# Performance work log

Hardware: AMD Instinct MI355X
Metric: run time of the kernel (lower is better)

The kernel has to match this reference:

```python
import jax, jax.numpy as jnp
import numpy as np

D = 256; NH = 8; DH = D // NH; NL = 4; NP = 4; DFFN = 1024
SPATIAL = [(128, 128), (64, 64), (32, 32), (16, 16)]
LEN_IN = sum(h * w for h, w in SPATIAL)
N, LQ = 8, 1000


def _ln(x, g, b, eps=1e-5):
    m = jnp.mean(x, -1, keepdims=True)
    v = jnp.mean((x - m) ** 2, -1, keepdims=True)
    return (x - m) * jax.lax.rsqrt(v + eps) * g + b


def _ms_deform_core(value, loc, attn_w):
    # value (N,Len_in,NH,DH); loc (N,Lq,NH,NL,NP,2) in [0,1]; attn_w (N,Lq,NH,NL,NP)
    n, lq = loc.shape[0], loc.shape[1]
    out = jnp.zeros((n, NH, lq, DH), value.dtype)
    start = 0
    for l, (Hl, Wl) in enumerate(SPATIAL):
        v = value[:, start:start + Hl * Wl].transpose(0, 2, 1, 3)  # (N,NH,HW,DH)
        start += Hl * Wl
        # grid_sample-style mapping, align_corners=False, zero padding
        x = loc[:, :, :, l, :, 0] * Wl - 0.5  # (N,Lq,NH,NP)
        y = loc[:, :, :, l, :, 1] * Hl - 0.5
        x0 = jnp.floor(x); y0 = jnp.floor(y)
        lx = x - x0; ly = y - y0
        x0i = x0.astype(jnp.int32); y0i = y0.astype(jnp.int32)
        acc = jnp.zeros((n, NH, lq, NP, DH), value.dtype)
        for dy, dx, w in ((0, 0, (1 - ly) * (1 - lx)), (0, 1, (1 - ly) * lx),
                          (1, 0, ly * (1 - lx)), (1, 1, ly * lx)):
            xi = x0i + dx; yi = y0i + dy
            valid = ((xi >= 0) & (xi < Wl) & (yi >= 0) & (yi < Hl)).astype(value.dtype)
            idx = jnp.clip(yi, 0, Hl - 1) * Wl + jnp.clip(xi, 0, Wl - 1)  # (N,Lq,NH,NP)
            idx = idx.transpose(0, 2, 1, 3).reshape(n, NH, lq * NP)
            g = jnp.take_along_axis(v, idx[..., None], axis=2).reshape(n, NH, lq, NP, DH)
            acc = acc + g * (w * valid).transpose(0, 2, 1, 3)[..., None]
        out = out + jnp.sum(acc * attn_w[:, :, :, l].transpose(0, 2, 1, 3)[..., None], axis=3)
    return out.transpose(0, 2, 1, 3).reshape(n, lq, D)


def setup_inputs() -> dict:
    key = jax.random.key(0)
    ks = jax.random.split(key, 16)
    s = 0.02
    inp = {
        'tgt': jax.random.normal(ks[0], (N, LQ, D), jnp.float32),
        'query_pos': jax.random.normal(ks[1], (N, LQ, D), jnp.float32),
        'reference_points': jax.random.uniform(ks[2], (N, LQ, NL, 2), jnp.float32),
        'src': jax.random.normal(ks[3], (N, LEN_IN, D), jnp.float32),
        'spatial_shapes': jnp.array(SPATIAL, jnp.int32),
        'level_start_index': jnp.array(np.cumsum([0] + [h * w for h, w in SPATIAL[:-1]]), jnp.int32),
        # self-attention
        'sa_in_w': jax.random.normal(ks[4], (3 * D, D), jnp.float32) * s,
        'sa_in_b': jnp.zeros((3 * D,), jnp.float32),
        'sa_out_w': jax.random.normal(ks[5], (D, D), jnp.float32) * s,
        'sa_out_b': jnp.zeros((D,), jnp.float32),
        'norm2_g': jnp.ones((D,), jnp.float32), 'norm2_b': jnp.zeros((D,), jnp.float32),
        # MSDeformAttn
        'off_w': jax.random.normal(ks[6], (NH * NL * NP * 2, D), jnp.float32) * s,
        'off_b': jax.random.normal(ks[7], (NH * NL * NP * 2,), jnp.float32) * s,
        'aw_w': jax.random.normal(ks[8], (NH * NL * NP, D), jnp.float32) * s,
        'aw_b': jnp.zeros((NH * NL * NP,), jnp.float32),
        'val_w': jax.random.normal(ks[9], (D, D), jnp.float32) * s,
        'val_b': jnp.zeros((D,), jnp.float32),
        'outp_w': jax.random.normal(ks[10], (D, D), jnp.float32) * s,
        'outp_b': jnp.zeros((D,), jnp.float32),
        'norm1_g': jnp.ones((D,), jnp.float32), 'norm1_b': jnp.zeros((D,), jnp.float32),
        # FFN
        'ffn_w1': jax.random.normal(ks[11], (DFFN, D), jnp.float32) * s,
        'ffn_b1': jnp.zeros((DFFN,), jnp.float32),
        'ffn_w2': jax.random.normal(ks[12], (D, DFFN), jnp.float32) * s,
        'ffn_b2': jnp.zeros((D,), jnp.float32),
        'norm3_g': jnp.ones((D,), jnp.float32), 'norm3_b': jnp.zeros((D,), jnp.float32),
    }
    return inp


def reference(tgt, query_pos, reference_points, src, spatial_shapes, level_start_index,
              sa_in_w, sa_in_b, sa_out_w, sa_out_b, norm2_g, norm2_b,
              off_w, off_b, aw_w, aw_b, val_w, val_b, outp_w, outp_b, norm1_g, norm1_b,
              ffn_w1, ffn_b1, ffn_w2, ffn_b2, norm3_g, norm3_b):
    n, lq, _ = tgt.shape
    # ---- self-attention (q = k = tgt + pos, v = tgt), eval mode (dropout off)
    qk = tgt + query_pos
    wq, wk, wv = sa_in_w[:D], sa_in_w[D:2 * D], sa_in_w[2 * D:]
    bq, bk, bv = sa_in_b[:D], sa_in_b[D:2 * D], sa_in_b[2 * D:]
    q = (qk @ wq.T + bq).reshape(n, lq, NH, DH)
    k = (qk @ wk.T + bk).reshape(n, lq, NH, DH)
    v = (tgt @ wv.T + bv).reshape(n, lq, NH, DH)
    scores = jnp.einsum('bqhd,bkhd->bhqk', q, k) / np.sqrt(DH).astype(np.float32)
    attn = jax.nn.softmax(scores, axis=-1)
    sa = jnp.einsum('bhqk,bkhd->bqhd', attn, v).reshape(n, lq, D) @ sa_out_w.T + sa_out_b
    tgt = _ln(tgt + sa, norm2_g, norm2_b)
    # ---- multi-scale deformable cross-attention
    query = tgt + query_pos
    value = (src @ val_w.T + val_b).reshape(n, LEN_IN, NH, DH)
    offsets = (query @ off_w.T + off_b).reshape(n, lq, NH, NL, NP, 2)
    aw = (query @ aw_w.T + aw_b).reshape(n, lq, NH, NL * NP)
    aw = jax.nn.softmax(aw, axis=-1).reshape(n, lq, NH, NL, NP)
    # offset normalizer: (W_l, H_l)
    norm = jnp.stack([spatial_shapes[:, 1], spatial_shapes[:, 0]], -1).astype(tgt.dtype)
    loc = reference_points[:, :, None, :, None, :] + offsets / norm[None, None, None, :, None, :]
    ca = _ms_deform_core(value, loc, aw) @ outp_w.T + outp_b
    tgt = _ln(tgt + ca, norm1_g, norm1_b)
    # ---- FFN
    ff = jax.nn.relu(tgt @ ffn_w1.T + ffn_b1) @ ffn_w2.T + ffn_b2
    tgt = _ln(tgt + ff, norm3_g, norm3_b)
    return tgt
```

## Files before the change

kernel.cpp:

```cpp
#include <hip/hip_runtime.h>
#include <hip/hip_bf16.h>

#define D 256
#define NH 8
#define DH 32
#define NL 4
#define NP 4
#define DFFN 1024
#define LEN_IN 21760
#define NB 8
#define LQ 1000

typedef __hip_bfloat16 bf16;
typedef __attribute__((ext_vector_type(8))) short s8v;
typedef __attribute__((ext_vector_type(4))) float f4v;

__device__ inline float toF(float x) { return x; }
__device__ inline float toF(bf16 x) { return __bfloat162float(x); }

template <typename T> __device__ inline T fromF(float x);
template <> __device__ inline float fromF<float>(float x) { return x; }
template <> __device__ inline bf16 fromF<bf16>(float x) { return __float2bfloat16(x); }

__device__ inline short bfr(float f) {
    unsigned u = __float_as_uint(f);
    u += 0x7fff + ((u >> 16) & 1);
    return (short)(u >> 16);
}
__device__ inline s8v pack8(float4 x, float4 y) {
    s8v r;
    r[0] = bfr(x.x); r[1] = bfr(x.y); r[2] = bfr(x.z); r[3] = bfr(x.w);
    r[4] = bfr(y.x); r[5] = bfr(y.y); r[6] = bfr(y.z); r[7] = bfr(y.w);
    return r;
}

template <typename TA, typename TC>
__global__ __launch_bounds__(256) void mfma_gemm(const TA* __restrict__ A, const float* __restrict__ A2,
                                                 const float* __restrict__ W, const float* __restrict__ bias,
                                                 TC* __restrict__ C, int M, int N, int K, int do_relu) {
    constexpr int LDT = 40;
    __shared__ bf16 As[128 * LDT];
    __shared__ bf16 Bs[128 * LDT];
    const int tid = threadIdx.x;
    const int m0 = blockIdx.y * 128, n0 = blockIdx.x * 128;
    const int srow = tid >> 1;
    const int sks = (tid & 1) * 16;
    const int lane = tid & 63;
    const int wave = tid >> 6;
    const int wm = (wave >> 1) * 64, wn = (wave & 1) * 64;
    const int fr = lane & 15, fq = lane >> 4;

    int arow = m0 + srow; if (arow >= M) arow = M - 1;
    const TA* aptr = A + (size_t)arow * K + sks;
    const float* a2ptr = A2 ? (A2 + (size_t)arow * K + sks) : nullptr;
    const float* wptr = W + (size_t)(n0 + srow) * K + sks;

    f4v acc[4][4];
#pragma unroll
    for (int i = 0; i < 4; ++i)
#pragma unroll
        for (int j = 0; j < 4; ++j) acc[i][j] = (f4v){0.f, 0.f, 0.f, 0.f};

    for (int k0 = 0; k0 < K; k0 += 32) {
        s8v av0, av1, wv0, wv1;
        if constexpr (sizeof(TA) == 2) {
            av0 = *(const s8v*)((const bf16*)aptr + k0);
            av1 = *(const s8v*)((const bf16*)aptr + k0 + 8);
        } else {
            float4 a0 = *(const float4*)(aptr + k0);
            float4 a1 = *(const float4*)(aptr + k0 + 4);
            float4 a2 = *(const float4*)(aptr + k0 + 8);
            float4 a3 = *(const float4*)(aptr + k0 + 12);
            if (a2ptr) {
                float4 b0 = *(const float4*)(a2ptr + k0);
                float4 b1 = *(const float4*)(a2ptr + k0 + 4);
                float4 b2 = *(const float4*)(a2ptr + k0 + 8);
                float4 b3 = *(const float4*)(a2ptr + k0 + 12);
                a0.x += b0.x; a0.y += b0.y; a0.z += b0.z; a0.w += b0.w;
                a1.x += b1.x; a1.y += b1.y; a1.z += b1.z; a1.w += b1.w;
                a2.x += b2.x; a2.y += b2.y; a2.z += b2.z; a2.w += b2.w;
                a3.x += b3.x; a3.y += b3.y; a3.z += b3.z; a3.w += b3.w;
            }
            av0 = pack8(a0, a1);
            av1 = pack8(a2, a3);
        }
        {
            float4 w0 = *(const float4*)(wptr + k0);
            float4 w1 = *(const float4*)(wptr + k0 + 4);
            float4 w2 = *(const float4*)(wptr + k0 + 8);
            float4 w3 = *(const float4*)(wptr + k0 + 12);
            wv0 = pack8(w0, w1);
            wv1 = pack8(w2, w3);
        }
        __syncthreads();
        *(s8v*)&As[srow * LDT + sks] = av0;
        *(s8v*)&As[srow * LDT + sks + 8] = av1;
        *(s8v*)&Bs[srow * LDT + sks] = wv0;
        *(s8v*)&Bs[srow * LDT + sks + 8] = wv1;
        __syncthreads();
        s8v af[4], bfv[4];
#pragma unroll
        for (int i = 0; i < 4; ++i) af[i] = *(s8v*)&As[(wm + i * 16 + fr) * LDT + fq * 8];
#pragma unroll
        for (int j = 0; j < 4; ++j) bfv[j] = *(s8v*)&Bs[(wn + j * 16 + fr) * LDT + fq * 8];
#pragma unroll
        for (int i = 0; i < 4; ++i)
#pragma unroll
            for (int j = 0; j < 4; ++j)
                acc[i][j] = __builtin_amdgcn_mfma_f32_16x16x32_bf16(af[i], bfv[j], acc[i][j], 0, 0, 0);
    }

#pragma unroll
    for (int i = 0; i < 4; ++i) {
        int rbase = m0 + wm + i * 16 + fq * 4;
#pragma unroll
        for (int r = 0; r < 4; ++r) {
            int row = rbase + r;
            if (row < M) {
#pragma unroll
                for (int j = 0; j < 4; ++j) {
                    int col = n0 + wn + j * 16 + fr;
                    float v = acc[i][j][r] + bias[col];
                    if (do_relu) v = fmaxf(v, 0.f);
                    C[(size_t)row * N + col] = fromF<TC>(v);
                }
            }
        }
    }
}

__global__ __launch_bounds__(256) void attn_mfma(const float* __restrict__ q, const float* __restrict__ k,
                                                 const float* __restrict__ v, float* __restrict__ out) {
    const int h = blockIdx.y, n = blockIdx.z;
    const int tid = threadIdx.x, wave = tid >> 6, lane = tid & 63;
    const int fr = lane & 15, fq = lane >> 4;
    __shared__ short Ks[32 * 40];
    __shared__ short Vt[32 * 40];
    __shared__ short Pl[4][16 * 40];
    const int q0 = blockIdx.x * 64 + wave * 16;

    s8v qfrag;
    {
        int qr = q0 + fr; if (qr >= LQ) qr = LQ - 1;
        const float* qp = q + ((size_t)(n * LQ + qr)) * D + h * DH + fq * 8;
        float4 t0 = *(const float4*)qp;
        float4 t1 = *(const float4*)(qp + 4);
        const float sc = 0.17677669529663687f;
        t0.x *= sc; t0.y *= sc; t0.z *= sc; t0.w *= sc;
        t1.x *= sc; t1.y *= sc; t1.z *= sc; t1.w *= sc;
        qfrag = pack8(t0, t1);
    }

    f4v O0 = {0.f, 0.f, 0.f, 0.f}, O1 = {0.f, 0.f, 0.f, 0.f};
    float mrow[4] = {-1e30f, -1e30f, -1e30f, -1e30f};
    float lrow[4] = {0.f, 0.f, 0.f, 0.f};

    for (int kt = 0; kt < LQ; kt += 32) {
        __syncthreads();
        {
            int key = tid >> 3, d4 = (tid & 7) * 4;
            int gk = kt + key; if (gk >= LQ) gk = LQ - 1;
            const float* kp = k + ((size_t)(n * LQ + gk)) * D + h * DH + d4;
            float4 t = *(const float4*)kp;
            short4 pk; pk.x = bfr(t.x); pk.y = bfr(t.y); pk.z = bfr(t.z); pk.w = bfr(t.w);
            *(short4*)&Ks[key * 40 + d4] = pk;
        }
        {
            int d = tid & 31, key0 = (tid >> 5) * 4;
            float vv[4];
#pragma unroll
            for (int i = 0; i < 4; ++i) {
                int gk = kt + key0 + i; if (gk >= LQ) gk = LQ - 1;
                vv[i] = v[((size_t)(n * LQ + gk)) * D + h * DH + d];
            }
            short4 pk; pk.x = bfr(vv[0]); pk.y = bfr(vv[1]); pk.z = bfr(vv[2]); pk.w = bfr(vv[3]);
            *(short4*)&Vt[d * 40 + key0] = pk;
        }
        __syncthreads();

        f4v s0 = {0.f, 0.f, 0.f, 0.f}, s1 = {0.f, 0.f, 0.f, 0.f};
        s8v kf0 = *(s8v*)&Ks[fr * 40 + fq * 8];
        s8v kf1 = *(s8v*)&Ks[(16 + fr) * 40 + fq * 8];
        s0 = __builtin_amdgcn_mfma_f32_16x16x32_bf16(qfrag, kf0, s0, 0, 0, 0);
        s1 = __builtin_amdgcn_mfma_f32_16x16x32_bf16(qfrag, kf1, s1, 0, 0, 0);
        const bool val0 = (kt + fr) < LQ, val1 = (kt + 16 + fr) < LQ;

        float p0[4], p1[4], alpha[4];
#pragma unroll
        for (int r = 0; r < 4; ++r) {
            float a = val0 ? s0[r] : -1e30f;
            float b = val1 ? s1[r] : -1e30f;
            float mx = fmaxf(a, b);
            mx = fmaxf(mx, __shfl_xor(mx, 1, 64));
            mx = fmaxf(mx, __shfl_xor(mx, 2, 64));
            mx = fmaxf(mx, __shfl_xor(mx, 4, 64));
            mx = fmaxf(mx, __shfl_xor(mx, 8, 64));
            float mnew = fmaxf(mrow[r], mx);
            float al = __expf(mrow[r] - mnew);
            float e0 = __expf(a - mnew);
            float e1 = __expf(b - mnew);
            float ps = e0 + e1;
            ps += __shfl_xor(ps, 1, 64);
            ps += __shfl_xor(ps, 2, 64);
            ps += __shfl_xor(ps, 4, 64);
            ps += __shfl_xor(ps, 8, 64);
            lrow[r] = lrow[r] * al + ps;
            mrow[r] = mnew;
            alpha[r] = al;
            p0[r] = e0; p1[r] = e1;
        }

        short* pw = Pl[wave];
#pragma unroll
        for (int r = 0; r < 4; ++r) {
            pw[(fq * 4 + r) * 40 + fr] = bfr(p0[r]);
            pw[(fq * 4 + r) * 40 + 16 + fr] = bfr(p1[r]);
        }
        __builtin_amdgcn_s_waitcnt(0);
        s8v pfrag = *(s8v*)&pw[fr * 40 + fq * 8];
        s8v vf0 = *(s8v*)&Vt[fr * 40 + fq * 8];
        s8v vf1 = *(s8v*)&Vt[(16 + fr) * 40 + fq * 8];
#pragma unroll
        for (int r = 0; r < 4; ++r) { O0[r] *= alpha[r]; O1[r] *= alpha[r]; }
        O0 = __builtin_amdgcn_mfma_f32_16x16x32_bf16(pfrag, vf0, O0, 0, 0, 0);
        O1 = __builtin_amdgcn_mfma_f32_16x16x32_bf16(pfrag, vf1, O1, 0, 0, 0);
    }

#pragma unroll
    for (int r = 0; r < 4; ++r) {
        int qrow = q0 + fq * 4 + r;
        if (qrow < LQ) {
            float inv = 1.0f / lrow[r];
            float* op = out + ((size_t)(n * LQ + qrow)) * D + h * DH;
            op[fr] = O0[r] * inv;
            op[16 + fr] = O1[r] * inv;
        }
    }
}

__global__ __launch_bounds__(256) void ln_res_kernel(const float* __restrict__ base, const float* __restrict__ delta,
                                                     const float* __restrict__ g, const float* __restrict__ b,
                                                     float* __restrict__ out) {
    __shared__ float scratch[8];
    const size_t row = blockIdx.x;
    const int d = threadIdx.x;
    float x = base[row * D + d] + delta[row * D + d];
    float s1 = x, s2 = x * x;
    for (int o = 32; o > 0; o >>= 1) {
        s1 += __shfl_down(s1, o, 64);
        s2 += __shfl_down(s2, o, 64);
    }
    const int w = threadIdx.x >> 6, lane = threadIdx.x & 63;
    if (lane == 0) { scratch[w] = s1; scratch[4 + w] = s2; }
    __syncthreads();
    s1 = scratch[0] + scratch[1] + scratch[2] + scratch[3];
    s2 = scratch[4] + scratch[5] + scratch[6] + scratch[7];
    float mean = s1 * (1.0f / 256.0f);
    float var = s2 * (1.0f / 256.0f) - mean * mean;
    float rstd = rsqrtf(var + 1e-5f);
    float y = (x - mean) * rstd * g[d] + b[d];
    out[row * D + d] = y;
}

__global__ __launch_bounds__(256) void aw_softmax_kernel(float* __restrict__ aw, int ngrp) {
    int t = blockIdx.x * 256 + threadIdx.x;
    if (t >= ngrp) return;
    float* p = aw + (size_t)t * 16;
    float m = p[0];
#pragma unroll
    for (int i = 1; i < 16; ++i) m = fmaxf(m, p[i]);
    float s = 0.f;
    float e[16];
#pragma unroll
    for (int i = 0; i < 16; ++i) { e[i] = __expf(p[i] - m); s += e[i]; }
    float inv = 1.0f / s;
#pragma unroll
    for (int i = 0; i < 16; ++i) p[i] = e[i] * inv;
}

__global__ __launch_bounds__(256) void deform_kernel(const bf16* __restrict__ value, const float* __restrict__ offs,
                                                     const float* __restrict__ aw, const float* __restrict__ refp,
                                                     float* __restrict__ out) {
    const int h = blockIdx.y, n = blockIdx.z;
    const int tid = threadIdx.x;
    const int wave = tid >> 6, lane = tid & 63;
    const int qi = blockIdx.x * 4 + wave;
    const int c = lane & 15;
    const int l = lane >> 4;
    const size_t row = (size_t)n * LQ + qi;
    const int W = 128 >> l, H = 128 >> l;
    const int START[4] = {0, 16384, 20480, 21504};
    const float invW = 1.0f / W, invH = 1.0f / H;

    const float rx = refp[(row * NL + l) * 2 + 0];
    const float ry = refp[(row * NL + l) * 2 + 1];
    const bf16* vbase = value + ((size_t)n * LEN_IN + START[l]) * D + h * DH + 2 * c;
    const float* offp = offs + row * D + (h * NL + l) * NP * 2;
    const float* awp = aw + row * 128 + h * 16 + l * 4;

    float acc0 = 0.f, acc1 = 0.f;
#pragma unroll
    for (int p = 0; p < 4; ++p) {
        float ox = offp[p * 2 + 0];
        float oy = offp[p * 2 + 1];
        float wa = awp[p];
        float x = (rx + ox * invW) * W - 0.5f;
        float y = (ry + oy * invH) * H - 0.5f;
        float xf = floorf(x), yf = floorf(y);
        float lx = x - xf, ly = y - yf;
        int x0 = (int)xf, y0 = (int)yf;
        int x1 = x0 + 1, y1 = y0 + 1;
        float vx0 = (x0 >= 0 && x0 < W) ? 1.f : 0.f;
        float vx1 = (x1 >= 0 && x1 < W) ? 1.f : 0.f;
        float vy0 = (y0 >= 0 && y0 < H) ? 1.f : 0.f;
        float vy1 = (y1 >= 0 && y1 < H) ? 1.f : 0.f;
        int x0c = min(max(x0, 0), W - 1), x1c = min(max(x1, 0), W - 1);
        int y0c = min(max(y0, 0), H - 1), y1c = min(max(y1, 0), H - 1);
        float w00 = wa * (1.f - ly) * (1.f - lx) * vy0 * vx0;
        float w01 = wa * (1.f - ly) * lx * vy0 * vx1;
        float w10 = wa * ly * (1.f - lx) * vy1 * vx0;
        float w11 = wa * ly * lx * vy1 * vx1;
        unsigned u00 = *(const unsigned*)(vbase + (size_t)(y0c * W + x0c) * D);
        unsigned u01 = *(const unsigned*)(vbase + (size_t)(y0c * W + x1c) * D);
        unsigned u10 = *(const unsigned*)(vbase + (size_t)(y1c * W + x0c) * D);
        unsigned u11 = *(const unsigned*)(vbase + (size_t)(y1c * W + x1c) * D);
        acc0 += w00 * __uint_as_float(u00 << 16) + w01 * __uint_as_float(u01 << 16)
              + w10 * __uint_as_float(u10 << 16) + w11 * __uint_as_float(u11 << 16);
        acc1 += w00 * __uint_as_float(u00 & 0xffff0000u) + w01 * __uint_as_float(u01 & 0xffff0000u)
              + w10 * __uint_as_float(u10 & 0xffff0000u) + w11 * __uint_as_float(u11 & 0xffff0000u);
    }
    acc0 += __shfl_xor(acc0, 16, 64); acc0 += __shfl_xor(acc0, 32, 64);
    acc1 += __shfl_xor(acc1, 16, 64); acc1 += __shfl_xor(acc1, 32, 64);
    if (l == 0) {
        float2 st = {acc0, acc1};
        *(float2*)(out + row * D + h * DH + 2 * c) = st;
    }
}

extern "C" void kernel_launch(void* const* d_in, const int* in_sizes, int n_in,
                              void* d_out, int out_size, void* d_ws, size_t ws_size,
                              hipStream_t stream) {
    const float* tgt = (const float*)d_in[0];
    const float* qpos = (const float*)d_in[1];
    const float* refp = (const float*)d_in[2];
    const float* src = (const float*)d_in[3];
    const float* sa_in_w = (const float*)d_in[6];
    const float* sa_in_b = (const float*)d_in[7];
    const float* sa_out_w = (const float*)d_in[8];
    const float* sa_out_b = (const float*)d_in[9];
    const float* norm2_g = (const float*)d_in[10];
    const float* norm2_b = (const float*)d_in[11];
    const float* off_w = (const float*)d_in[12];
    const float* off_b = (const float*)d_in[13];
    const float* aw_w = (const float*)d_in[14];
    const float* aw_b = (const float*)d_in[15];
    const float* val_w = (const float*)d_in[16];
    const float* val_b = (const float*)d_in[17];
    const float* outp_w = (const float*)d_in[18];
    const float* outp_b = (const float*)d_in[19];
    const float* norm1_g = (const float*)d_in[20];
    const float* norm1_b = (const float*)d_in[21];
    const float* ffn_w1 = (const float*)d_in[22];
    const float* ffn_b1 = (const float*)d_in[23];
    const float* ffn_w2 = (const float*)d_in[24];
    const float* ffn_b2 = (const float*)d_in[25];
    const float* norm3_g = (const float*)d_in[26];
    const float* norm3_b = (const float*)d_in[27];
    float* outp = (float*)d_out;

    const size_t NTOK = (size_t)NB * LQ;
    const size_t NE = NTOK * D;
    float* w = (float*)d_ws;
    size_t off = 0;
    auto alloc = [&](size_t n) { float* p = w + off; off += n; return p; };
    float* bufA = alloc(NE);
    float* bufB = alloc(NE);
    float* bufC = alloc(NE);
    float* bufD = alloc(NE);
    float* tgt2 = alloc(NE);
    float* tgt3 = alloc(NE);
    float* awb = alloc(NTOK * 128);
    bf16* mid = (bf16*)alloc(NTOK * DFFN / 2);
    bf16* value = (bf16*)(w + off);

    const int M8K = (int)NTOK;
    dim3 gD(2, (M8K + 127) / 128);

    mfma_gemm<float, float><<<gD, 256, 0, stream>>>(tgt, qpos, sa_in_w, sa_in_b, bufB, M8K, D, D, 0);
    mfma_gemm<float, float><<<gD, 256, 0, stream>>>(tgt, qpos, sa_in_w + 256 * 256, sa_in_b + 256, bufC, M8K, D, D, 0);
    mfma_gemm<float, float><<<gD, 256, 0, stream>>>(tgt, nullptr, sa_in_w + 512 * 256, sa_in_b + 512, bufD, M8K, D, D, 0);
    attn_mfma<<<dim3((LQ + 63) / 64, NH, NB), 256, 0, stream>>>(bufB, bufC, bufD, bufA);
    mfma_gemm<float, float><<<gD, 256, 0, stream>>>(bufA, nullptr, sa_out_w, sa_out_b, bufB, M8K, D, D, 0);
    ln_res_kernel<<<NTOK, 256, 0, stream>>>(tgt, bufB, norm2_g, norm2_b, tgt2);

    mfma_gemm<float, bf16><<<dim3(2, (NB * LEN_IN) / 128), 256, 0, stream>>>(src, nullptr, val_w, val_b, value,
                                                                             NB * LEN_IN, D, D, 0);
    mfma_gemm<float, float><<<gD, 256, 0, stream>>>(tgt2, qpos, off_w, off_b, bufD, M8K, D, D, 0);
    mfma_gemm<float, float><<<dim3(1, (M8K + 127) / 128), 256, 0, stream>>>(tgt2, qpos, aw_w, aw_b, awb, M8K, 128, D, 0);
    aw_softmax_kernel<<<(int)(NTOK * NH + 255) / 256, 256, 0, stream>>>(awb, (int)(NTOK * NH));
    deform_kernel<<<dim3(LQ / 4, NH, NB), 256, 0, stream>>>(value, bufD, awb, refp, bufA);
    mfma_gemm<float, float><<<gD, 256, 0, stream>>>(bufA, nullptr, outp_w, outp_b, bufB, M8K, D, D, 0);
    ln_res_kernel<<<NTOK, 256, 0, stream>>>(tgt2, bufB, norm1_g, norm1_b, tgt3);

    mfma_gemm<float, bf16><<<dim3(DFFN / 128, (M8K + 127) / 128), 256, 0, stream>>>(tgt3, nullptr, ffn_w1, ffn_b1,
                                                                                    mid, M8K, DFFN, D, 1);
    mfma_gemm<bf16, float><<<gD, 256, 0, stream>>>(mid, nullptr, ffn_w2, ffn_b2, bufC, M8K, D, DFFN, 0);
    ln_res_kernel<<<NTOK, 256, 0, stream>>>(tgt3, bufC, norm3_g, norm3_b, outp);
}
```

Baseline: 691.2 us.

## Pre-pack weights to bf16 and replace LDS-tiled GEMM with direct-load MFMA GEMM

A new kernel converts all fp32 weight matrices to bf16 in one launch at the start of the forward pass. The GEMM kernel is rewritten to load A and W fragments straight from global memory into MFMA registers, with no shared-memory staging or barriers. It uses a hardware packed bf16 convert and smaller 64-row tiles so more blocks launch. This removes LDS traffic and syncs, but gives up on-chip data reuse and drops the M-bound guards, relying on M being a multiple of 64.

```diff
diff --git a/kernel.cpp b/kernel.cpp
--- a/kernel.cpp
+++ b/kernel.cpp
@@ -15,9 +15,6 @@
 typedef __attribute__((ext_vector_type(8))) short s8v;
 typedef __attribute__((ext_vector_type(4))) float f4v;
 
-__device__ inline float toF(float x) { return x; }
-__device__ inline float toF(bf16 x) { return __bfloat162float(x); }
-
 template <typename T> __device__ inline T fromF(float x);
 template <> __device__ inline float fromF<float>(float x) { return x; }
 template <> __device__ inline bf16 fromF<bf16>(float x) { return __float2bfloat16(x); }
@@ -34,96 +31,112 @@
     return r;
 }
 
-template <typename TA, typename TC>
-__global__ __launch_bounds__(256) void mfma_gemm(const TA* __restrict__ A, const float* __restrict__ A2,
-                                                 const float* __restrict__ W, const float* __restrict__ bias,
-                                                 TC* __restrict__ C, int M, int N, int K, int do_relu) {
-    constexpr int LDT = 40;
-    __shared__ bf16 As[128 * LDT];
-    __shared__ bf16 Bs[128 * LDT];
+__device__ inline unsigned cvtpk(float a, float b) {
+    unsigned r;
+    asm("v_cvt_pk_bf16_f32 %0, %1, %2" : "=v"(r) : "v"(a), "v"(b));
+    return r;
+}
+__device__ inline s8v pkcvt8(float4 a, float4 b) {
+    union { s8v v; unsigned u[4]; } r;
+    r.u[0] = cvtpk(a.x, a.y);
+    r.u[1] = cvtpk(a.z, a.w);
+    r.u[2] = cvtpk(b.x, b.y);
+    r.u[3] = cvtpk(b.z, b.w);
+    return r.v;
+}
+
+__global__ __launch_bounds__(256) void pack_weights(const float* __restrict__ s0, const float* __restrict__ s1,
+                                                    const float* __restrict__ s2, const float* __restrict__ s3,
+                                                    const float* __restrict__ s4, const float* __restrict__ s5,
+                                                    const float* __restrict__ s6, const float* __restrict__ s7,
+                                                    bf16* __restrict__ dst) {
+    int g = blockIdx.x * 256 + threadIdx.x;
+    const float* s; int base;
+    if      (g <  49152) { s = s0; base = 0;      }
+    else if (g <  65536) { s = s1; base = 49152;  }
+    else if (g <  81920) { s = s2; base = 65536;  }
+    else if (g <  90112) { s = s3; base = 81920;  }
+    else if (g < 106496) { s = s4; base = 90112;  }
+    else if (g < 122880) { s = s5; base = 106496; }
+    else if (g < 188416) { s = s6; base = 122880; }
+    else                 { s = s7; base = 188416; }
+    float4 v = ((const float4*)s)[g - base];
+    short4 o; o.x = bfr(v.x); o.y = bfr(v.y); o.z = bfr(v.z); o.w = bfr(v.w);
+    ((short4*)dst)[g] = o;
+}
+
+template <typename TA, typename TC, int MT, bool ADD2>
+__global__ __launch_bounds__(256) void gemm_direct(const TA* __restrict__ A, const float* __restrict__ A2,
+                                                   const bf16* __restrict__ W, const float* __restrict__ bias,
+                                                   TC* __restrict__ C, int M, int N, int K, int do_relu) {
     const int tid = threadIdx.x;
-    const int m0 = blockIdx.y * 128, n0 = blockIdx.x * 128;
-    const int srow = tid >> 1;
-    const int sks = (tid & 1) * 16;
-    const int lane = tid & 63;
-    const int wave = tid >> 6;
-    const int wm = (wave >> 1) * 64, wn = (wave & 1) * 64;
+    const int lane = tid & 63, wave = tid >> 6;
     const int fr = lane & 15, fq = lane >> 4;
-
-    int arow = m0 + srow; if (arow >= M) arow = M - 1;
-    const TA* aptr = A + (size_t)arow * K + sks;
-    const float* a2ptr = A2 ? (A2 + (size_t)arow * K + sks) : nullptr;
-    const float* wptr = W + (size_t)(n0 + srow) * K + sks;
-
-    f4v acc[4][4];
-#pragma unroll
-    for (int i = 0; i < 4; ++i)
+    const int n0 = blockIdx.x * 128;
+    const int wrow = blockIdx.y * (MT * 32) + (wave >> 1) * (MT * 16);
+    const int wn = n0 + (wave & 1) * 64;
+    (void)M;
+
+    const TA* ap[MT];
+    const float* a2p[MT];
+#pragma unroll
+    for (int i = 0; i < MT; ++i) {
+        size_t r = (size_t)(wrow + i * 16 + fr);
+        ap[i] = A + r * K + fq * 8;
+        if constexpr (ADD2) a2p[i] = A2 + r * K + fq * 8;
+    }
+    const bf16* wp[4];
+#pragma unroll
+    for (int j = 0; j < 4; ++j) wp[j] = W + (size_t)(wn + j * 16 + fr) * K + fq * 8;
+
+    f4v acc[MT][4];
+#pragma unroll
+    for (int i = 0; i < MT; ++i)
 #pragma unroll
         for (int j = 0; j < 4; ++j) acc[i][j] = (f4v){0.f, 0.f, 0.f, 0.f};
 
     for (int k0 = 0; k0 < K; k0 += 32) {
-        s8v av0, av1, wv0, wv1;
-        if constexpr (sizeof(TA) == 2) {
-            av0 = *(const s8v*)((const bf16*)aptr + k0);
-            av1 = *(const s8v*)((const bf16*)aptr + k0 + 8);
-        } else {
-            float4 a0 = *(const float4*)(aptr + k0);
-            float4 a1 = *(const float4*)(aptr + k0 + 4);
-            float4 a2 = *(const float4*)(aptr + k0 + 8);
-            float4 a3 = *(const float4*)(aptr + k0 + 12);
-            if (a2ptr) {
-                float4 b0 = *(const float4*)(a2ptr + k0);
-                float4 b1 = *(const float4*)(a2ptr + k0 + 4);
-                float4 b2 = *(const float4*)(a2ptr + k0 + 8);
-                float4 b3 = *(const float4*)(a2ptr + k0 + 12);
-                a0.x += b0.x; a0.y += b0.y; a0.z += b0.z; a0.w += b0.w;
-                a1.x += b1.x; a1.y += b1.y; a1.z += b1.z; a1.w += b1.w;
-                a2.x += b2.x; a2.y += b2.y; a2.z += b2.z; a2.w += b2.w;
-                a3.x += b3.x; a3.y += b3.y; a3.z += b3.z; a3.w += b3.w;
+        s8v bfv[4];
+#pragma unroll
+        for (int j = 0; j < 4; ++j) { bfv[j] = *(const s8v*)wp[j]; wp[j] += 32; }
+        s8v af[MT];
+#pragma unroll
+        for (int i = 0; i < MT; ++i) {
+            if constexpr (sizeof(TA) == 2) {
+                af[i] = *(const s8v*)ap[i];
+            } else {
+                float4 x0 = *(const float4*)ap[i];
+                float4 x1 = *(const float4*)(ap[i] + 4);
+                if constexpr (ADD2) {
+                    float4 y0 = *(const float4*)a2p[i];
+                    float4 y1 = *(const float4*)(a2p[i] + 4);
+                    x0.x += y0.x; x0.y += y0.y; x0.z += y0.z; x0.w += y0.w;
+                    x1.x += y1.x; x1.y += y1.y; x1.z += y1.z; x1.w += y1.w;
+                    a2p[i] += 32;
+                }
+                af[i] = pkcvt8(x0, x1);
             }
-            av0 = pack8(a0, a1);
-            av1 = pack8(a2, a3);
-        }
-        {
-            float4 w0 = *(const float4*)(wptr + k0);
-            float4 w1 = *(const float4*)(wptr + k0 + 4);
-            float4 w2 = *(const float4*)(wptr + k0 + 8);
-            float4 w3 = *(const float4*)(wptr + k0 + 12);
-            wv0 = pack8(w0, w1);
-            wv1 = pack8(w2, w3);
-        }
-        __syncthreads();
-        *(s8v*)&As[srow * LDT + sks] = av0;
-        *(s8v*)&As[srow * LDT + sks + 8] = av1;
-        *(s8v*)&Bs[srow * LDT + sks] = wv0;
-        *(s8v*)&Bs[srow * LDT + sks + 8] = wv1;
-        __syncthreads();
-        s8v af[4], bfv[4];
-#pragma unroll
-        for (int i = 0; i < 4; ++i) af[i] = *(s8v*)&As[(wm + i * 16 + fr) * LDT + fq * 8];
-#pragma unroll
-        for (int j = 0; j < 4; ++j) bfv[j] = *(s8v*)&Bs[(wn + j * 16 + fr) * LDT + fq * 8];
-#pragma unroll
-        for (int i = 0; i < 4; ++i)
+            ap[i] += 32;
+        }
+#pragma unroll
+        for (int i = 0; i < MT; ++i)
 #pragma unroll
             for (int j = 0; j < 4; ++j)
                 acc[i][j] = __builtin_amdgcn_mfma_f32_16x16x32_bf16(af[i], bfv[j], acc[i][j], 0, 0, 0);
     }
 
 #pragma unroll
-    for (int i = 0; i < 4; ++i) {
-        int rbase = m0 + wm + i * 16 + fq * 4;
-#pragma unroll
-        for (int r = 0; r < 4; ++r) {
-            int row = rbase + r;
-            if (row < M) {
-#pragma unroll
-                for (int j = 0; j < 4; ++j) {
-                    int col = n0 + wn + j * 16 + fr;
-                    float v = acc[i][j][r] + bias[col];
-                    if (do_relu) v = fmaxf(v, 0.f);
-                    C[(size_t)row * N + col] = fromF<TC>(v);
-                }
+    for (int j = 0; j < 4; ++j) {
+        const int col = wn + j * 16 + fr;
+        const float bb = bias[col];
+#pragma unroll
+        for (int i = 0; i < MT; ++i) {
+            const int rbase = wrow + i * 16 + fq * 4;
+#pragma unroll
+            for (int r = 0; r < 4; ++r) {
+                float v = acc[i][j][r] + bb;
+                if (do_relu) v = fmaxf(v, 0.f);
+                C[(size_t)(rbase + r) * N + col] = fromF<TC>(v);
             }
         }
     }
@@ -381,29 +394,45 @@
     float* tgt3 = alloc(NE);
     float* awb = alloc(NTOK * 128);
     bf16* mid = (bf16*)alloc(NTOK * DFFN / 2);
-    bf16* value = (bf16*)(w + off);
+    bf16* value = (bf16*)alloc((size_t)NB * LEN_IN * D / 2);
+    bf16* wb = (bf16*)alloc(507904);
+
+    const bf16* wq    = wb;
+    const bf16* wk    = wb + 65536;
+    const bf16* wv    = wb + 131072;
+    const bf16* wo    = wb + 196608;
+    const bf16* woff  = wb + 262144;
+    const bf16* waw   = wb + 327680;
+    const bf16* wval  = wb + 360448;
+    const bf16* woutp = wb + 425984;
+    const bf16* wf1   = wb + 491520;
+    const bf16* wf2   = wb + 753664;
 
     const int M8K = (int)NTOK;
-    dim3 gD(2, (M8K + 127) / 128);
-
-    mfma_gemm<float, float><<<gD, 256, 0, stream>>>(tgt, qpos, sa_in_w, sa_in_b, bufB, M8K, D, D, 0);
-    mfma_gemm<float, float><<<gD, 256, 0, stream>>>(tgt, qpos, sa_in_w + 256 * 256, sa_in_b + 256, bufC, M8K, D, D, 0);
-    mfma_gemm<float, float><<<gD, 256, 0, stream>>>(tgt, nullptr, sa_in_w + 512 * 256, sa_in_b + 512, bufD, M8K, D, D, 0);
+    dim3 g8(2, M8K / 64);
+    dim3 g8aw(1, M8K / 64);
+    dim3 g8f1(DFFN / 128, M8K / 64);
+    dim3 gVal(2, (NB * LEN_IN) / 128);
+
+    pack_weights<<<992, 256, 0, stream>>>(sa_in_w, sa_out_w, off_w, aw_w, val_w, outp_w, ffn_w1, ffn_w2, wb);
+
+    gemm_direct<float, float, 2, true><<<g8, 256, 0, stream>>>(tgt, qpos, wq, sa_in_b, bufB, M8K, D, D, 0);
+    gemm_direct<float, float, 2, true><<<g8, 256, 0, stream>>>(tgt, qpos, wk, sa_in_b + 256, bufC, M8K, D, D, 0);
+    gemm_direct<float, float, 2, false><<<g8, 256, 0, stream>>>(tgt, nullptr, wv, sa_in_b + 512, bufD, M8K, D, D, 0);
     attn_mfma<<<dim3((LQ + 63) / 64, NH, NB), 256, 0, stream>>>(bufB, bufC, bufD, bufA);
-    mfma_gemm<float, float><<<gD, 256, 0, stream>>>(bufA, nullptr, sa_out_w, sa_out_b, bufB, M8K, D, D, 0);
+    gemm_direct<float, float, 2, false><<<g8, 256, 0, stream>>>(bufA, nullptr, wo, sa_out_b, bufB, M8K, D, D, 0);
     ln_res_kernel<<<NTOK, 256, 0, stream>>>(tgt, bufB, norm2_g, norm2_b, tgt2);
 
-    mfma_gemm<float, bf16><<<dim3(2, (NB * LEN_IN) / 128), 256, 0, stream>>>(src, nullptr, val_w, val_b, value,
-                                                                             NB * LEN_IN, D, D, 0);
-    mfma_gemm<float, float><<<gD, 256, 0, stream>>>(tgt2, qpos, off_w, off_b, bufD, M8K, D, D, 0);
-    mfma_gemm<float, float><<<dim3(1, (M8K + 127) / 128), 256, 0, stream>>>(tgt2, qpos, aw_w, aw_b, awb, M8K, 128, D, 0);
+    gemm_direct<float, bf16, 4, false><<<gVal, 256, 0, stream>>>(src, nullptr, wval, val_b, value,
+                                                                 NB * LEN_IN, D, D, 0);
+    gemm_direct<float, float, 2, true><<<g8, 256, 0, stream>>>(tgt2, qpos, woff, off_b, bufD, M8K, D, D, 0);
+    gemm_direct<float, float, 2, true><<<g8aw, 256, 0, stream>>>(tgt2, qpos, waw, aw_b, awb, M8K, 128, D, 0);
     aw_softmax_kernel<<<(int)(NTOK * NH + 255) / 256, 256, 0, stream>>>(awb, (int)(NTOK * NH));
     deform_kernel<<<dim3(LQ / 4, NH, NB), 256, 0, stream>>>(value, bufD, awb, refp, bufA);
-    mfma_gemm<float, float><<<gD, 256, 0, stream>>>(bufA, nullptr, outp_w, outp_b, bufB, M8K, D, D, 0);
+    gemm_direct<float, float, 2, false><<<g8, 256, 0, stream>>>(bufA, nullptr, woutp, outp_b, bufB, M8K, D, D, 0);
     ln_res_kernel<<<NTOK, 256, 0, stream>>>(tgt2, bufB, norm1_g, norm1_b, tgt3);
 
-    mfma_gemm<float, bf16><<<dim3(DFFN / 128, (M8K + 127) / 128), 256, 0, stream>>>(tgt3, nullptr, ffn_w1, ffn_b1,
-                                                                                    mid, M8K, DFFN, D, 1);
-    mfma_gemm<bf16, float><<<gD, 256, 0, stream>>>(mid, nullptr, ffn_w2, ffn_b2, bufC, M8K, D, DFFN, 0);
+    gemm_direct<float, bf16, 2, false><<<g8f1, 256, 0, stream>>>(tgt3, nullptr, wf1, ffn_b1, mid, M8K, DFFN, D, 1);
+    gemm_direct<bf16, float, 2, false><<<g8, 256, 0, stream>>>(mid, nullptr, wf2, ffn_b2, bufC, M8K, D, DFFN, 0);
     ln_res_kernel<<<NTOK, 256, 0, stream>>>(tgt3, bufC, norm3_g, norm3_b, outp);
 }
```

After: 699.2 us. No clear change (+1.2%).
